# Kernel tuning notes

Hardware: AMD Instinct MI355X
Metric: run time of the kernel (lower is better)

## Reference

```python
import jax, jax.numpy as jnp
import numpy as np

D_MODEL = 1024
NUM_HEADS = 16
D_K = D_MODEL // NUM_HEADS


def setup_inputs() -> dict:
    key = jax.random.key(0)
    k1, k2, k3, k4 = jax.random.split(key, 4)
    x = jax.random.normal(k1, (2, 2048, D_MODEL), dtype=jnp.float32)
    # qkv_proj: Linear(d_model, 3*d_model, bias=False); stored as [in, out] for x @ W
    W_qkv = jax.random.normal(k2, (D_MODEL, 3 * D_MODEL), dtype=jnp.float32) * (1.0 / np.sqrt(D_MODEL))
    W_out = jax.random.normal(k3, (D_MODEL, D_MODEL), dtype=jnp.float32) * (1.0 / np.sqrt(D_MODEL))
    b_out = jax.random.normal(k4, (D_MODEL,), dtype=jnp.float32) * 0.01
    return {"x": x, "W_qkv": W_qkv, "W_out": W_out, "b_out": b_out}


def reference(x, W_qkv, W_out, b_out):
    B, N, C = x.shape
    scale = 1.0 / np.sqrt(D_K)
    qkv = (x @ W_qkv).reshape(B, N, 3, NUM_HEADS, D_K)
    qkv = jnp.transpose(qkv, (2, 0, 3, 1, 4))  # [3, B, H, N, d_k]
    q, k, v = qkv[0], qkv[1], qkv[2]
    scores = jnp.einsum("bhqd,bhkd->bhqk", q, k) * scale  # [B,H,N,N]
    attn = jax.nn.softmax(scores, axis=-1)
    out = jnp.einsum("bhqk,bhkd->bhqd", attn, v)  # [B,H,N,d_k]
    out = jnp.transpose(out, (0, 2, 1, 3)).reshape(B, N, C)
    return out @ W_out + b_out
```

## Files before the change

kernel.cpp:

```cpp
#include <hip/hip_runtime.h>
#include <cstdint>

typedef __bf16 bf16_t;
typedef __bf16 bf16x8 __attribute__((ext_vector_type(8)));
typedef float  f32x4  __attribute__((ext_vector_type(4)));
typedef uint32_t u32x4 __attribute__((ext_vector_type(4)));

#define MFMA16(a,b,c) __builtin_amdgcn_mfma_f32_16x16x32_bf16((a),(b),(c),0,0,0)

__device__ __forceinline__ void gload_lds16(const bf16_t* g, bf16_t* l) {
  __builtin_amdgcn_global_load_lds(
      (const __attribute__((address_space(1))) unsigned int*)g,
      (__attribute__((address_space(3))) unsigned int*)l,
      16, 0, 0);
}

__device__ __forceinline__ uint32_t cvt_pk_bf16(float lo, float hi) {
  uint32_t r;
  asm("v_cvt_pk_bf16_f32 %0, %1, %2" : "=v"(r) : "v"(lo), "v"(hi));
  return r;
}

__global__ void k_conv_x(const float* __restrict__ x, bf16_t* __restrict__ xb) {
  int i = blockIdx.x * blockDim.x + threadIdx.x;
  const float4* p = reinterpret_cast<const float4*>(x) + (size_t)i * 2;
  float4 a = p[0], b = p[1];
  bf16x8 v;
  v[0]=(bf16_t)a.x; v[1]=(bf16_t)a.y; v[2]=(bf16_t)a.z; v[3]=(bf16_t)a.w;
  v[4]=(bf16_t)b.x; v[5]=(bf16_t)b.y; v[6]=(bf16_t)b.z; v[7]=(bf16_t)b.w;
  *reinterpret_cast<bf16x8*>(xb + (size_t)i * 8) = v;
}

__global__ void k_transpose_w(const float* __restrict__ W, bf16_t* __restrict__ WT,
                              int K, int N) {
  __shared__ float tile[32][33];
  int n0 = blockIdx.x * 32, k0 = blockIdx.y * 32;
  int c = threadIdx.x & 31, r8 = threadIdx.x >> 5;
#pragma unroll
  for (int rr = 0; rr < 4; rr++) {
    int r = r8 + rr * 8;
    tile[r][c] = W[(size_t)(k0 + r) * N + n0 + c];
  }
  __syncthreads();
#pragma unroll
  for (int rr = 0; rr < 4; rr++) {
    int r = r8 + rr * 8;
    WT[(size_t)(n0 + r) * K + k0 + c] = (bf16_t)tile[c][r];
  }
}

__global__ void k_vtrans(const bf16_t* __restrict__ V, bf16_t* __restrict__ VT) {
  __shared__ bf16_t t[64 * 72];
  int bi = blockIdx.x;
  int head = bi >> 5, kt = bi & 31;
  int tid = threadIdx.x;
  const bf16_t* src = V + (size_t)head * 131072 + (size_t)kt * 64 * 64;
#pragma unroll
  for (int j = 0; j < 2; j++) {
    int q = tid + 256 * j;
    int key = q >> 3, part = q & 7;
    bf16x8 v = *reinterpret_cast<const bf16x8*>(src + key * 64 + part * 8);
    *reinterpret_cast<bf16x8*>(&t[key * 72 + part * 8]) = v;
  }
  __syncthreads();
  bf16_t* dst = VT + (size_t)head * 131072 + kt * 64;
#pragma unroll
  for (int j = 0; j < 2; j++) {
    int q = tid + 256 * j;
    int dv = q >> 3, part = q & 7;
    bf16x8 v;
#pragma unroll
    for (int e = 0; e < 8; e++) v[e] = t[(part * 8 + e) * 72 + dv];
    *reinterpret_cast<bf16x8*>(dst + (size_t)dv * 2048 + part * 8) = v;
  }
}

#define BAR()    __builtin_amdgcn_s_barrier()
#define LGKM0()  do { asm volatile("s_waitcnt lgkmcnt(0)" ::: "memory"); \
                      __builtin_amdgcn_sched_barrier(0); } while (0)
#define VMW(n)   asm volatile("s_waitcnt vmcnt(" #n ")" ::: "memory")

#define LDA(buf, mh) do {                                                   \
    char* base_ = L + ((buf) * 2 + wr) * 16384;                             \
    _Pragma("unroll")                                                       \
    for (int mf = 0; mf < 4; mf++) {                                        \
      int r_ = ((mh) * 64 + mf * 16 + li) * 128;                            \
      a[mf][0] = *reinterpret_cast<const bf16x8*>(base_ + r_ + aoff0);      \
      a[mf][1] = *reinterpret_cast<const bf16x8*>(base_ + r_ + aoff1);      \
    } } while (0)

#define LDB(buf, nh) do {                                                   \
    char* base_ = L + 65536 + ((buf) * 2 + (wc >> 1)) * 16384;              \
    _Pragma("unroll")                                                       \
    for (int nf = 0; nf < 2; nf++) {                                        \
      int r_ = (((wc & 1) * 64) + (nh) * 32 + nf * 16 + li) * 128;          \
      b[nh][nf][0] = *reinterpret_cast<const bf16x8*>(base_ + r_ + aoff0);  \
      b[nh][nf][1] = *reinterpret_cast<const bf16x8*>(base_ + r_ + aoff1);  \
    } } while (0)

#define QUAD(mh, nh) do {                                                   \
    __builtin_amdgcn_s_setprio(1);                                          \
    _Pragma("unroll")                                                       \
    for (int mf = 0; mf < 4; mf++)                                          \
      _Pragma("unroll")                                                     \
      for (int nf = 0; nf < 2; nf++) {                                      \
        acc[mh][nh][mf][nf] = MFMA16(a[mf][0], b[nh][nf][0], acc[mh][nh][mf][nf]); \
        acc[mh][nh][mf][nf] = MFMA16(a[mf][1], b[nh][nf][1], acc[mh][nh][mf][nf]); \
      }                                                                      \
    __builtin_amdgcn_s_setprio(0); } while (0)

__global__ __launch_bounds__(512, 2) void k_gemm_qkv(
    const bf16_t* __restrict__ A, const bf16_t* __restrict__ BT, int Klen,
    bf16_t* __restrict__ Qo, bf16_t* __restrict__ Ko, bf16_t* __restrict__ Vo) {
  extern __shared__ bf16_t lds[];
  int tid = threadIdx.x, lane = tid & 63, wid = tid >> 6;
  int wr = wid >> 2, wc = wid & 3;
  int g = lane >> 4, li = lane & 15;

  int lin = (blockIdx.x & 7) * 24 + (blockIdx.x >> 3);
  int bx = lin & 15, by = lin >> 4;
  int row0 = bx * 256, col0 = by * 256;

  char* L = (char*)lds;
  int sw    = (li & 7) << 4;
  int aoff0 = (g * 16) ^ sw;
  int aoff1 = (g * 16 + 64) ^ sw;
  int soff_e = ((((tid & 7) * 16) ^ (((tid >> 3) & 7) << 4))) >> 1;

  f32x4 acc[2][2][4][2] = {};
  bf16x8 a[4][2], b[2][2][2];

  int nk = Klen >> 6;

  auto stageA = [&](int h, int kt) {
    int rb = row0 + h * 128 + (tid >> 3);
    const bf16_t* src = A + (size_t)rb * Klen + kt * 64 + soff_e;
    bf16_t* dst = lds + ((kt & 1) * 2 + h) * 8192 + tid * 8;
    gload_lds16(src, dst);
    gload_lds16(src + (size_t)64 * Klen, dst + 4096);
  };
  auto stageB = [&](int h, int kt) {
    int rb = col0 + h * 128 + (tid >> 3);
    const bf16_t* src = BT + (size_t)rb * Klen + kt * 64 + soff_e;
    bf16_t* dst = lds + 32768 + ((kt & 1) * 2 + h) * 8192 + tid * 8;
    gload_lds16(src, dst);
    gload_lds16(src + (size_t)64 * Klen, dst + 4096);
  };

  stageA(0, 0); stageA(1, 0); stageB(0, 0); stageB(1, 0);
  stageB(0, 1); stageB(1, 1);
  VMW(4); BAR();

  for (int i = 0; i < nk / 2; i++) {
    int T1 = 2 * i + 1, T2 = 2 * i + 2, T3 = 2 * i + 3;
    bool s2 = T2 < nk, s3 = T3 < nk;
    LDA(0, 0); LDB(0, 0); stageA(0, T1);
    BAR(); LGKM0(); QUAD(0, 0); BAR();
    LDB(0, 1); stageA(1, T1);
    BAR(); LGKM0(); QUAD(0, 1); BAR();
    LDA(0, 1); if (s2) stageB(0, T2);
    BAR(); LGKM0(); QUAD(1, 0); BAR();
    if (s2) stageB(1, T2);
    BAR(); QUAD(1, 1);
    if (s2) { VMW(4); } else { VMW(0); }
    BAR();
    LDA(1, 0); LDB(1, 0); if (s2) stageA(0, T2);
    BAR(); LGKM0(); QUAD(0, 0); BAR();
    LDB(1, 1); if (s2) stageA(1, T2);
    BAR(); LGKM0(); QUAD(0, 1); BAR();
    LDA(1, 1); if (s3) stageB(0, T3);
    BAR(); LGKM0(); QUAD(1, 0); BAR();
    if (s3) stageB(1, T3);
    BAR(); QUAD(1, 1);
    if (s3) { VMW(4); } else { VMW(0); }
    BAR();
  }

#pragma unroll
  for (int mh = 0; mh < 2; mh++)
#pragma unroll
    for (int nh = 0; nh < 2; nh++)
#pragma unroll
      for (int mf = 0; mf < 4; mf++)
#pragma unroll
        for (int nf = 0; nf < 2; nf++) {
          int rg = row0 + wr * 128 + mh * 64 + mf * 16 + g * 4;
          int cg = col0 + wc * 64 + nh * 32 + nf * 16 + li;
          int t = cg >> 10, h = (cg >> 6) & 15, dk = cg & 63;
#pragma unroll
          for (int ii = 0; ii < 4; ii++) {
            float v = acc[mh][nh][mf][nf][ii];
            int row = rg + ii;
            int b2 = row >> 11, nn = row & 2047;
            size_t idx = ((size_t)((b2 << 4) + h) * 2048 + nn) * 64 + dk;
            if (t == 0)      Qo[idx] = (bf16_t)(v * 0.18033688011112042f);
            else if (t == 1) Ko[idx] = (bf16_t)v;
            else             Vo[idx] = (bf16_t)v;
          }
        }
}

template<int EPI, int MT>
__global__ __launch_bounds__(256, 2) void k_gemm(
    const bf16_t* __restrict__ A, const bf16_t* __restrict__ BT, int Klen,
    bf16_t* __restrict__ Qo, bf16_t* __restrict__ Ko, bf16_t* __restrict__ Vo,
    const float* __restrict__ bias, float* __restrict__ Out, int Nout) {
  constexpr int WM = MT / 2;
  constexpr int MF = WM / 16;
  __shared__ bf16_t As[2][MT * 32];
  __shared__ bf16_t Bs[2][4096];
  int tid = threadIdx.x, lane = tid & 63, wid = tid >> 6;
  int row0 = blockIdx.x * MT, col0 = blockIdx.y * 128;
  int wr = wid >> 1, wc = wid & 1;
  int g = lane >> 4, li = lane & 15;

  f32x4 acc[MF][4] = {};

  auto stage = [&](int buf, int kt) {
    int k0 = kt * 32;
#pragma unroll
    for (int j = 0; j < MT / 64; j++) {
      int q = tid + 256 * j;
      int r = q >> 2, part = q & 3;
      gload_lds16(A + (size_t)(row0 + r) * Klen + k0 + part * 8,
                  &As[buf][q * 8]);
    }
#pragma unroll
    for (int j = 0; j < 2; j++) {
      int q = tid + 256 * j;
      int r = q >> 2, part = q & 3;
      gload_lds16(BT + (size_t)(col0 + r) * Klen + k0 + part * 8,
                  &Bs[buf][q * 8]);
    }
  };

  int nk = Klen >> 5;
  stage(0, 0);
  for (int kt = 0; kt < nk; kt++) {
    __syncthreads();
    if (kt + 1 < nk) stage((kt + 1) & 1, kt + 1);
    int buf = kt & 1;
    int kl = g * 8;
    bf16x8 a[MF], b[4];
#pragma unroll
    for (int m = 0; m < MF; m++)
      a[m] = *reinterpret_cast<const bf16x8*>(&As[buf][(wr * WM + m * 16 + li) * 32 + kl]);
#pragma unroll
    for (int n = 0; n < 4; n++)
      b[n] = *reinterpret_cast<const bf16x8*>(&Bs[buf][(wc * 64 + n * 16 + li) * 32 + kl]);
#pragma unroll
    for (int m = 0; m < MF; m++)
#pragma unroll
      for (int n = 0; n < 4; n++)
        acc[m][n] = MFMA16(a[m], b[n], acc[m][n]);
  }

#pragma unroll
  for (int m = 0; m < MF; m++) {
    int rg = row0 + wr * WM + m * 16 + g * 4;
#pragma unroll
    for (int n = 0; n < 4; n++) {
      int cg = col0 + wc * 64 + n * 16 + li;
#pragma unroll
      for (int i = 0; i < 4; i++) {
        float v = acc[m][n][i];
        int row = rg + i;
        if constexpr (EPI == 0) {
          int t = cg >> 10, h = (cg >> 6) & 15, dk = cg & 63;
          int b2 = row >> 11, nn = row & 2047;
          size_t idx = ((size_t)((b2 << 4) + h) * 2048 + nn) * 64 + dk;
          if (t == 0)      Qo[idx] = (bf16_t)(v * 0.18033688011112042f);
          else if (t == 1) Ko[idx] = (bf16_t)v;
          else             Vo[idx] = (bf16_t)v;
        } else {
          Out[(size_t)row * Nout + cg] = v + bias[cg];
        }
      }
    }
  }
}

__global__ __launch_bounds__(256, 2) void k_flash(
    const bf16_t* __restrict__ Q, const bf16_t* __restrict__ K,
    const bf16_t* __restrict__ VT, bf16_t* __restrict__ O) {
  __shared__ bf16_t Ks[2][64 * 64];
  __shared__ bf16_t Vs[2][64 * 64];

  int bi = (blockIdx.x & 7) * 64 + (blockIdx.x >> 3);
  int head = bi >> 4, qt = bi & 15;
  int tid = threadIdx.x, lane = tid & 63, wid = tid >> 6;
  int g = lane >> 4, li = lane & 15;

  const bf16_t* Qh = Q + (size_t)head * 131072 + (size_t)qt * 128 * 64;
  const bf16_t* Kh = K + (size_t)head * 131072;
  const bf16_t* Vh = VT + (size_t)head * 131072;

  bf16x8 qf[2][2];
#pragma unroll
  for (int rg = 0; rg < 2; rg++) {
    const bf16_t* qrow = Qh + (size_t)(wid * 32 + rg * 16 + li) * 64;
    qf[rg][0] = *reinterpret_cast<const bf16x8*>(qrow + g * 8);
    qf[rg][1] = *reinterpret_cast<const bf16x8*>(qrow + 32 + g * 8);
  }

  u32x4 onesw;
  onesw[0] = 0x3F803F80u; onesw[1] = 0x3F803F80u;
  onesw[2] = 0x3F803F80u; onesw[3] = 0x3F803F80u;
  bf16x8 ones = __builtin_bit_cast(bf16x8, onesw);

  f32x4 o[2][4] = {};
  f32x4 osum[2] = {};
  float mrun[2] = {0.f, 0.f};

  auto stage = [&](int buf, int t) {
    int kv0 = t * 64;
#pragma unroll
    for (int j = 0; j < 2; j++) {
      int q = tid + 256 * j;
      int key = q >> 3, part = q & 7;
      int sw = (key & 7) ^ (((key >> 3) & 3) << 1);
      gload_lds16(Kh + (size_t)(kv0 + key) * 64 + ((part ^ sw) * 8),
                  &Ks[buf][(tid + j * 256) * 8]);
    }
#pragma unroll
    for (int j = 0; j < 2; j++) {
      int q = tid + 256 * j;
      int dv = q >> 3, part = q & 7;
      gload_lds16(Vh + (size_t)dv * 2048 + kv0 + ((part ^ (dv & 7)) * 8),
                  &Vs[buf][(tid + j * 256) * 8]);
    }
  };

  stage(0, 0);
  for (int t = 0; t < 32; t++) {
    __syncthreads();
    if (t + 1 < 32) stage((t + 1) & 1, t + 1);
    int buf = t & 1;
    char* KsB = (char*)&Ks[buf][0];
    char* VsB = (char*)&Vs[buf][0];

    bf16x8 ka[2][4];
#pragma unroll
    for (int kd = 0; kd < 2; kd++)
#pragma unroll
      for (int nf = 0; nf < 4; nf++) {
        int key = ((li >> 2) << 3) | ((nf & 1) << 2) | (li & 3) | ((nf >> 1) << 5);
        int sw = (key & 7) ^ (((key >> 3) & 3) << 1);
        ka[kd][nf] = *reinterpret_cast<const bf16x8*>(
            KsB + key * 128 + (((kd * 4 + g) ^ sw) << 4));
      }

    f32x4 s[2][4];
#pragma unroll
    for (int rg = 0; rg < 2; rg++) {
      float nm = -mrun[rg];
#pragma unroll
      for (int nf = 0; nf < 4; nf++) {
        s[rg][nf][0] = nm; s[rg][nf][1] = nm; s[rg][nf][2] = nm; s[rg][nf][3] = nm;
      }
    }
    __builtin_amdgcn_s_setprio(1);
#pragma unroll
    for (int kd = 0; kd < 2; kd++)
#pragma unroll
      for (int nf = 0; nf < 4; nf++) {
        s[0][nf] = MFMA16(ka[kd][nf], qf[0][kd], s[0][nf]);
        s[1][nf] = MFMA16(ka[kd][nf], qf[1][kd], s[1][nf]);
      }
    __builtin_amdgcn_s_setprio(0);

    float pmax[2];
#pragma unroll
    for (int rg = 0; rg < 2; rg++) {
      float t0 = fmaxf(fmaxf(s[rg][0][0], s[rg][0][1]), s[rg][0][2]);
      float t1 = fmaxf(fmaxf(s[rg][0][3], s[rg][1][0]), s[rg][1][1]);
      float t2 = fmaxf(fmaxf(s[rg][1][2], s[rg][1][3]), s[rg][2][0]);
      float t3 = fmaxf(fmaxf(s[rg][2][1], s[rg][2][2]), s[rg][2][3]);
      float t4 = fmaxf(fmaxf(s[rg][3][0], s[rg][3][1]), s[rg][3][2]);
      pmax[rg] = fmaxf(fmaxf(fmaxf(t0, t1), fmaxf(t2, t3)), fmaxf(t4, s[rg][3][3]));
    }

    bool ok = (pmax[0] <= 8.f) & (pmax[1] <= 8.f);
    if (!__all(ok)) {
#pragma unroll
      for (int rg = 0; rg < 2; rg++) {
        float v = pmax[rg];
        v = fmaxf(v, __shfl_xor(v, 16));
        v = fmaxf(v, __shfl_xor(v, 32));
        float d = fmaxf(v, 0.f);
        float sc = __builtin_amdgcn_exp2f(-d);
        mrun[rg] += d;
#pragma unroll
        for (int nf = 0; nf < 4; nf++)
#pragma unroll
          for (int i = 0; i < 4; i++) s[rg][nf][i] -= d;
        float osc[4];
#pragma unroll
        for (int i = 0; i < 4; i++) osc[i] = __shfl(sc, g * 4 + i);
#pragma unroll
        for (int nf = 0; nf < 4; nf++)
#pragma unroll
          for (int i = 0; i < 4; i++) o[rg][nf][i] *= osc[i];
#pragma unroll
        for (int i = 0; i < 4; i++) osum[rg][i] *= osc[i];
      }
    }

    bf16x8 pa[2][2];
#pragma unroll
    for (int rg = 0; rg < 2; rg++) {
#pragma unroll
      for (int nf = 0; nf < 4; nf++)
#pragma unroll
        for (int i = 0; i < 4; i++)
          s[rg][nf][i] = __builtin_amdgcn_exp2f(s[rg][nf][i]);
      u32x4 w0, w1;
      w0[0] = cvt_pk_bf16(s[rg][0][0], s[rg][0][1]);
      w0[1] = cvt_pk_bf16(s[rg][0][2], s[rg][0][3]);
      w0[2] = cvt_pk_bf16(s[rg][1][0], s[rg][1][1]);
      w0[3] = cvt_pk_bf16(s[rg][1][2], s[rg][1][3]);
      w1[0] = cvt_pk_bf16(s[rg][2][0], s[rg][2][1]);
      w1[1] = cvt_pk_bf16(s[rg][2][2], s[rg][2][3]);
      w1[2] = cvt_pk_bf16(s[rg][3][0], s[rg][3][1]);
      w1[3] = cvt_pk_bf16(s[rg][3][2], s[rg][3][3]);
      pa[rg][0] = __builtin_bit_cast(bf16x8, w0);
      pa[rg][1] = __builtin_bit_cast(bf16x8, w1);
    }

    __builtin_amdgcn_s_setprio(1);
    osum[0] = MFMA16(pa[0][0], ones, osum[0]);
    osum[0] = MFMA16(pa[0][1], ones, osum[0]);
    osum[1] = MFMA16(pa[1][0], ones, osum[1]);
    osum[1] = MFMA16(pa[1][1], ones, osum[1]);
#pragma unroll
    for (int nfv = 0; nfv < 4; nfv++) {
      int dv = nfv * 16 + li;
      bf16x8 b0 = *reinterpret_cast<const bf16x8*>(
          VsB + dv * 128 + ((g * 16) ^ ((dv & 7) << 4)));
      bf16x8 b1 = *reinterpret_cast<const bf16x8*>(
          VsB + dv * 128 + ((64 + g * 16) ^ ((dv & 7) << 4)));
      o[0][nfv] = MFMA16(pa[0][0], b0, o[0][nfv]);
      o[0][nfv] = MFMA16(pa[0][1], b1, o[0][nfv]);
      o[1][nfv] = MFMA16(pa[1][0], b0, o[1][nfv]);
      o[1][nfv] = MFMA16(pa[1][1], b1, o[1][nfv]);
    }
    __builtin_amdgcn_s_setprio(0);
  }

  int b2 = head >> 4, h = head & 15;
#pragma unroll
  for (int rg = 0; rg < 2; rg++) {
#pragma unroll
    for (int i = 0; i < 4; i++) {
      float inv = 1.f / osum[rg][i];
      int n = qt * 128 + wid * 32 + rg * 16 + g * 4 + i;
      size_t base = ((size_t)b2 * 2048 + n) * 1024 + h * 64;
#pragma unroll
      for (int nfv = 0; nfv < 4; nfv++)
        O[base + nfv * 16 + li] = (bf16_t)(o[rg][nfv][i] * inv);
    }
  }
}

extern "C" void kernel_launch(void* const* d_in, const int* in_sizes, int n_in,
                              void* d_out, int out_size, void* d_ws, size_t ws_size,
                              hipStream_t stream) {
  const float* x    = (const float*)d_in[0];
  const float* Wqkv = (const float*)d_in[1];
  const float* Wout = (const float*)d_in[2];
  const float* bout = (const float*)d_in[3];
  float* out = (float*)d_out;

  char* ws = (char*)d_ws;
  bf16_t* xb    = (bf16_t*)(ws);
  bf16_t* wqkvT = (bf16_t*)(ws + ((size_t)8  << 20));
  bf16_t* woutT = (bf16_t*)(ws + ((size_t)14 << 20));
  bf16_t* qw    = (bf16_t*)(ws + ((size_t)16 << 20));
  bf16_t* kw    = (bf16_t*)(ws + ((size_t)24 << 20));
  bf16_t* vw    = (bf16_t*)(ws + ((size_t)32 << 20));
  bf16_t* vtw   = (bf16_t*)(ws + ((size_t)40 << 20));
  bf16_t* ow    = (bf16_t*)(ws + ((size_t)48 << 20));

  static bool attr_set = false;
  if (!attr_set) {
    hipFuncSetAttribute((const void*)k_gemm_qkv,
                        hipFuncAttributeMaxDynamicSharedMemorySize, 131072);
    attr_set = true;
  }

  k_conv_x<<<2048, 256, 0, stream>>>(x, xb);
  k_transpose_w<<<dim3(96, 32), 256, 0, stream>>>(Wqkv, wqkvT, 1024, 3072);
  k_transpose_w<<<dim3(32, 32), 256, 0, stream>>>(Wout, woutT, 1024, 1024);
  k_gemm_qkv<<<192, 512, 131072, stream>>>(xb, wqkvT, 1024, qw, kw, vw);
  k_vtrans<<<1024, 256, 0, stream>>>(vw, vtw);
  k_flash<<<512, 256, 0, stream>>>(qw, kw, vtw, ow);
  k_gemm<1,64><<<dim3(64, 8), 256, 0, stream>>>(ow, woutT, 1024,
                                                nullptr, nullptr, nullptr,
                                                bout, out, 1024);
}
```

Baseline: 117.6 us.

## Split flash attention across two KV halves and merge partial results

Splits each query tile's key/value range into two halves processed by separate blocks, doubling the grid to 1024 blocks and raising the occupancy hint. Each block writes normalized partial outputs plus row max and sum, and a new merge kernel combines them with log-sum-exp weights into the final layout. This targets the underfilled GPU with 512 blocks, at the cost of extra global traffic for partials, a second kernel launch, and bf16 rounding of the partial outputs. It also drops the static guard on the shared-memory attribute call, so that call now runs on every launch.

```diff
diff --git a/kernel.cpp b/kernel.cpp
--- a/kernel.cpp
+++ b/kernel.cpp
@@ -280,14 +280,16 @@
   }
 }
 
-__global__ __launch_bounds__(256, 2) void k_flash(
+__global__ __launch_bounds__(256, 4) void k_flashp(
     const bf16_t* __restrict__ Q, const bf16_t* __restrict__ K,
-    const bf16_t* __restrict__ VT, bf16_t* __restrict__ O) {
+    const bf16_t* __restrict__ VT,
+    bf16_t* __restrict__ po0, bf16_t* __restrict__ po1,
+    float* __restrict__ pm, float* __restrict__ pl) {
   __shared__ bf16_t Ks[2][64 * 64];
   __shared__ bf16_t Vs[2][64 * 64];
 
-  int bi = (blockIdx.x & 7) * 64 + (blockIdx.x >> 3);
-  int head = bi >> 4, qt = bi & 15;
+  int bi = (blockIdx.x & 7) * 128 + (blockIdx.x >> 3);
+  int head = bi >> 5, qt = (bi >> 1) & 15, kv = bi & 1;
   int tid = threadIdx.x, lane = tid & 63, wid = tid >> 6;
   int g = lane >> 4, li = lane & 15;
 
@@ -313,7 +315,7 @@
   float mrun[2] = {0.f, 0.f};
 
   auto stage = [&](int buf, int t) {
-    int kv0 = t * 64;
+    int kv0 = (kv * 16 + t) * 64;
 #pragma unroll
     for (int j = 0; j < 2; j++) {
       int q = tid + 256 * j;
@@ -332,9 +334,9 @@
   };
 
   stage(0, 0);
-  for (int t = 0; t < 32; t++) {
+  for (int t = 0; t < 16; t++) {
     __syncthreads();
-    if (t + 1 < 32) stage((t + 1) & 1, t + 1);
+    if (t + 1 < 16) stage((t + 1) & 1, t + 1);
     int buf = t & 1;
     char* KsB = (char*)&Ks[buf][0];
     char* VsB = (char*)&Vs[buf][0];
@@ -447,18 +449,68 @@
     __builtin_amdgcn_s_setprio(0);
   }
 
-  int b2 = head >> 4, h = head & 15;
+  bf16_t* po = kv ? po1 : po0;
+  size_t pbase = (size_t)(head * 16 + qt) * 128 * 64;
 #pragma unroll
   for (int rg = 0; rg < 2; rg++) {
 #pragma unroll
     for (int i = 0; i < 4; i++) {
       float inv = 1.f / osum[rg][i];
-      int n = qt * 128 + wid * 32 + rg * 16 + g * 4 + i;
-      size_t base = ((size_t)b2 * 2048 + n) * 1024 + h * 64;
+      int r = wid * 32 + rg * 16 + g * 4 + i;
 #pragma unroll
       for (int nfv = 0; nfv < 4; nfv++)
-        O[base + nfv * 16 + li] = (bf16_t)(o[rg][nfv][i] * inv);
-    }
+        po[pbase + (size_t)r * 64 + nfv * 16 + li] = (bf16_t)(o[rg][nfv][i] * inv);
+    }
+  }
+  float rowm[2][4];
+#pragma unroll
+  for (int rg = 0; rg < 2; rg++)
+#pragma unroll
+    for (int i = 0; i < 4; i++)
+      rowm[rg][i] = __shfl(mrun[rg], g * 4 + i);
+  if (li == 0) {
+    size_t sbase = (size_t)(kv * 512 + head * 16 + qt) * 128;
+#pragma unroll
+    for (int rg = 0; rg < 2; rg++)
+#pragma unroll
+      for (int i = 0; i < 4; i++) {
+        int r = wid * 32 + rg * 16 + g * 4 + i;
+        pm[sbase + r] = rowm[rg][i];
+        pl[sbase + r] = osum[rg][i];
+      }
+  }
+}
+
+__global__ __launch_bounds__(256) void k_merge(
+    const bf16_t* __restrict__ po0, const bf16_t* __restrict__ po1,
+    const float* __restrict__ pm, const float* __restrict__ pl,
+    bf16_t* __restrict__ O) {
+  int blk = blockIdx.x;
+  int head = blk >> 4, qt = blk & 15;
+  int b2 = head >> 4, h = head & 15;
+  int tid = threadIdx.x;
+  int colg = tid & 7, rq = tid >> 3;
+#pragma unroll
+  for (int r8 = 0; r8 < 4; r8++) {
+    int r = r8 * 32 + rq;
+    size_t si = (size_t)blk * 128 + r;
+    float ma = pm[si], mb = pm[si + 512 * 128];
+    float la = pl[si], lb = pl[si + 512 * 128];
+    float mm = fmaxf(ma, mb);
+    float za = la * __builtin_amdgcn_exp2f(ma - mm);
+    float zb = lb * __builtin_amdgcn_exp2f(mb - mm);
+    float inv = 1.f / (za + zb);
+    float wa = za * inv, wb = zb * inv;
+    size_t pidx = ((size_t)blk * 128 + r) * 64 + colg * 8;
+    bf16x8 va = *reinterpret_cast<const bf16x8*>(po0 + pidx);
+    bf16x8 vb = *reinterpret_cast<const bf16x8*>(po1 + pidx);
+    bf16x8 vo;
+#pragma unroll
+    for (int e = 0; e < 8; e++)
+      vo[e] = (bf16_t)((float)va[e] * wa + (float)vb[e] * wb);
+    int n = qt * 128 + r;
+    *reinterpret_cast<bf16x8*>(
+        O + ((size_t)b2 * 2048 + n) * 1024 + h * 64 + colg * 8) = vo;
   }
 }
 
@@ -480,20 +532,21 @@
   bf16_t* vw    = (bf16_t*)(ws + ((size_t)32 << 20));
   bf16_t* vtw   = (bf16_t*)(ws + ((size_t)40 << 20));
   bf16_t* ow    = (bf16_t*)(ws + ((size_t)48 << 20));
-
-  static bool attr_set = false;
-  if (!attr_set) {
-    hipFuncSetAttribute((const void*)k_gemm_qkv,
-                        hipFuncAttributeMaxDynamicSharedMemorySize, 131072);
-    attr_set = true;
-  }
+  bf16_t* po0   = (bf16_t*)(ws);
+  bf16_t* po1   = (bf16_t*)(ws + ((size_t)32 << 20));
+  float*  pm    = (float*)(ws + ((size_t)8  << 20));
+  float*  pl    = (float*)(ws + ((size_t)9  << 20));
+
+  hipFuncSetAttribute((const void*)k_gemm_qkv,
+                      hipFuncAttributeMaxDynamicSharedMemorySize, 131072);
 
   k_conv_x<<<2048, 256, 0, stream>>>(x, xb);
   k_transpose_w<<<dim3(96, 32), 256, 0, stream>>>(Wqkv, wqkvT, 1024, 3072);
   k_transpose_w<<<dim3(32, 32), 256, 0, stream>>>(Wout, woutT, 1024, 1024);
   k_gemm_qkv<<<192, 512, 131072, stream>>>(xb, wqkvT, 1024, qw, kw, vw);
   k_vtrans<<<1024, 256, 0, stream>>>(vw, vtw);
-  k_flash<<<512, 256, 0, stream>>>(qw, kw, vtw, ow);
+  k_flashp<<<1024, 256, 0, stream>>>(qw, kw, vtw, po0, po1, pm, pl);
+  k_merge<<<512, 256, 0, stream>>>(po0, po1, pm, pl, ow);
   k_gemm<1,64><<<dim3(64, 8), 256, 0, stream>>>(ow, woutT, 1024,
                                                 nullptr, nullptr, nullptr,
                                                 bout, out, 1024);
```

Measured after the change: 127.0 us. +8.0%, slower.
